# Optimization experiments

Measured on AMD Instinct MI355X. Metric: run time of the kernel, lower is better.

Reference implementation:

```python
import jax, jax.numpy as jnp
import numpy as np

D_HEAD = 64
NEG_INF = jnp.float32(-jnp.inf)


def setup_inputs() -> dict:
    key = jax.random.key(0)
    ks = jax.random.split(key, 6)
    B, S, D, N, H = 8, 1024, 768, 12, 64
    init = 0.02
    return {
        "normalized_resid_pre": jax.random.normal(ks[0], (B, S, D), jnp.float32),
        "W_Q": jax.random.normal(ks[1], (N, D, H), jnp.float32) * init,
        "W_K": jax.random.normal(ks[2], (N, D, H), jnp.float32) * init,
        "W_V": jax.random.normal(ks[3], (N, D, H), jnp.float32) * init,
        "W_O": jax.random.normal(ks[4], (N, H, D), jnp.float32) * init,
        "b_Q": jnp.zeros((N, H), jnp.float32),
        "b_K": jnp.zeros((N, H), jnp.float32),
        "b_V": jnp.zeros((N, H), jnp.float32),
        "b_O": jnp.zeros((D,), jnp.float32),
    }


def _causal_mask(attn_scores):
    # Faithful to the source: keep entries where triu(scores, 1) != scores
    # (i.e. lower triangle incl. diagonal), set the rest to -inf.
    return jnp.where(jnp.triu(attn_scores, k=1) != attn_scores, attn_scores, NEG_INF)


def reference(normalized_resid_pre, W_Q, W_K, W_V, W_O, b_Q, b_K, b_V, b_O):
    x = normalized_resid_pre  # [b, p, d]
    keys = jnp.einsum('bpd,ndh->bpnh', x, W_K) + b_K
    queries = jnp.einsum('bpd,ndh->bpnh', x, W_Q) + b_Q
    attn_scores = jnp.einsum('bknh,bqnh->bnqk', keys, queries)  # [b, n, s_q, s_k]
    attn_probs = jax.nn.softmax(_causal_mask(attn_scores / np.sqrt(D_HEAD)), axis=-1)
    values = jnp.einsum('bpd,ndh->bpnh', x, W_V) + b_V
    z = jnp.einsum('bknh,bnqk->bqnh', values, attn_probs)
    attn_out = jnp.einsum('bpnh,nhe->bpe', z, W_O) + b_O
    return attn_out
```

## Files before the change

kernel.cpp:

```cpp
#include <hip/hip_runtime.h>
#include <stdint.h>

typedef __attribute__((ext_vector_type(4))) float f32x4;
typedef __attribute__((ext_vector_type(8))) __bf16 bf16v8;
typedef __attribute__((ext_vector_type(8))) unsigned short u16x8;
typedef __attribute__((ext_vector_type(4))) unsigned short u16x4;
typedef unsigned short u16;

#define AS1 __attribute__((address_space(1)))
#define AS3 __attribute__((address_space(3)))

__device__ __forceinline__ u16 f2b(float f) {
  union { __bf16 h; u16 u; } c; c.h = (__bf16)f; return c.u;
}

__device__ __forceinline__ f32x4 mfma16(bf16v8 a, bf16v8 b, f32x4 c) {
  return __builtin_amdgcn_mfma_f32_16x16x32_bf16(a, b, c, 0, 0, 0);
}

__device__ __forceinline__ void gl_lds16(const void* g, void* l) {
  __builtin_amdgcn_global_load_lds((AS1 void*)g, (AS3 void*)l, 16, 0, 0);
}

__global__ __launch_bounds__(256) void pack_x_kernel(
    const float* __restrict__ x, u16* __restrict__ xb, int n8) {
  int i = blockIdx.x * 256 + threadIdx.x;
  if (i >= n8) return;
  const f32x4* p = (const f32x4*)(x + (size_t)i * 8);
  f32x4 a = p[0], b = p[1];
  u16x8 o;
  o[0] = f2b(a[0]); o[1] = f2b(a[1]); o[2] = f2b(a[2]); o[3] = f2b(a[3]);
  o[4] = f2b(b[0]); o[5] = f2b(b[1]); o[6] = f2b(b[2]); o[7] = f2b(b[3]);
  *(u16x8*)(xb + (size_t)i * 8) = o;
}

__global__ __launch_bounds__(256) void pack_w_kernel(
    const float* __restrict__ in, u16* __restrict__ out,
    int in_ns, int in_rs, int out_ns, int out_rs, float scale) {
  __shared__ float t[64][65];
  const int n = blockIdx.z;
  const int a0 = blockIdx.x * 64, b0 = blockIdx.y * 64;
  const int c = threadIdx.x & 63, w = threadIdx.x >> 6;
  const float* ip = in + (size_t)n * in_ns;
#pragma unroll
  for (int i = 0; i < 16; ++i) {
    int r = i * 4 + w;
    t[r][c] = ip[(size_t)(a0 + r) * in_rs + (b0 + c)];
  }
  __syncthreads();
  u16* op = out + (size_t)n * out_ns;
#pragma unroll
  for (int i = 0; i < 16; ++i) {
    int r = i * 4 + w;
    op[(size_t)(b0 + r) * out_rs + (a0 + c)] = f2b(t[c][r] * scale);
  }
}

__global__ __launch_bounds__(256) void pack_bias_kernel(
    const float* __restrict__ bq, const float* __restrict__ bk,
    float* __restrict__ o, float sq) {
  int i = blockIdx.x * 256 + threadIdx.x;
  if (i < 768) o[i] = bq[i] * sq;
  else if (i < 1536) o[i] = bk[i - 768];
}

template <int OUTF32, int BIASROW>
__global__ __launch_bounds__(256, 2) void gemm_bt(
    const u16* __restrict__ A, const u16* __restrict__ Bt,
    void* __restrict__ Cv, const float* __restrict__ bias, float scale, int N) {
  constexpr int K = 768;
  __shared__ u16 lA[2][128 * 32];
  __shared__ u16 lB[2][128 * 32];

  const int tid = threadIdx.x;
  const int lane = tid & 63, wid = tid >> 6;
  const int wr = wid >> 1, wc = wid & 1;
  const int g = lane >> 4, l16 = lane & 15;
  const int m0 = blockIdx.x * 128, n0 = blockIdx.y * 128;

  const int srow = tid >> 2;
  const int scol = (tid & 3) * 16;

  f32x4 acc[4][4];
#pragma unroll
  for (int i = 0; i < 4; ++i)
#pragma unroll
    for (int j = 0; j < 4; ++j) acc[i][j] = (f32x4)0.f;

  const char* Ab = (const char*)(A + (size_t)m0 * K);
  const char* Bb = (const char*)(Bt + (size_t)n0 * K);
  char* lAb = (char*)&lA[0][0];
  char* lBb = (char*)&lB[0][0];

#define STAGE(buf, kt)                                                          \
  do {                                                                          \
    int kb = (kt) * 64;                                                         \
    gl_lds16(Ab + (size_t)srow * 1536 + kb + scol,                              \
             lAb + (buf) * 8192 + wid * 1024);                                  \
    gl_lds16(Bb + (size_t)srow * 1536 + kb + scol,                              \
             lBb + (buf) * 8192 + wid * 1024);                                  \
    gl_lds16(Ab + (size_t)(64 + srow) * 1536 + kb + scol,                       \
             lAb + (buf) * 8192 + 4096 + wid * 1024);                           \
    gl_lds16(Bb + (size_t)(64 + srow) * 1536 + kb + scol,                       \
             lBb + (buf) * 8192 + 4096 + wid * 1024);                           \
  } while (0)

  STAGE(0, 0);
  __syncthreads();

  for (int kt = 0; kt < 24; ++kt) {
    const int cur = kt & 1;
    if (kt + 1 < 24) STAGE(cur ^ 1, kt + 1);
    bf16v8 af[4], bfv[4];
#pragma unroll
    for (int i = 0; i < 4; ++i) {
      af[i]  = *(const bf16v8*)&lA[cur][(wr * 64 + i * 16 + l16) * 32 + g * 8];
      bfv[i] = *(const bf16v8*)&lB[cur][(wc * 64 + i * 16 + l16) * 32 + g * 8];
    }
#pragma unroll
    for (int i = 0; i < 4; ++i)
#pragma unroll
      for (int j = 0; j < 4; ++j)
        acc[i][j] = mfma16(af[i], bfv[j], acc[i][j]);
    __syncthreads();
  }
#undef STAGE

  const int row0 = m0 + wr * 64, col0 = n0 + wc * 64;
#pragma unroll
  for (int j = 0; j < 4; ++j) {
    const int col = col0 + j * 16 + l16;
    const float bcol = BIASROW ? 0.f : bias[col];
#pragma unroll
    for (int i = 0; i < 4; ++i) {
#pragma unroll
      for (int r = 0; r < 4; ++r) {
        const int row = row0 + i * 16 + g * 4 + r;
        const float bv = BIASROW ? bias[row] : bcol;
        const float v = (acc[i][j][r] + bv) * scale;
        if (OUTF32) ((float*)Cv)[(size_t)row * N + col] = v;
        else        ((u16*)Cv)[(size_t)row * N + col] = f2b(v);
      }
    }
  }
}

__global__ __launch_bounds__(256, 3) void flash6_kernel(
    const u16* __restrict__ QK, const u16* __restrict__ Vt,
    u16* __restrict__ Z) {
  __shared__ u16 lK[2][64 * 64];
  __shared__ u16 lV[2][64 * 64];
  __shared__ u16 lP[64 * 72];

  const int tid = threadIdx.x;
  const int lane = tid & 63, wid = tid >> 6;
  const int g = lane >> 4, l16 = lane & 15;

  const int id = blockIdx.x;
  const int xs = id & 7;
  const int rest = id >> 3;
  const int p = rest & 7;
  const int j = rest >> 3;
  const int head = xs + 8 * j;
  const int b = head / 12, n = head % 12;

  const int nchA = 16 - p;
  const int total = 17;

  const u16* Qh = QK + (size_t)b * 1024 * 1536 + n * 64;
  const u16* Kh = Qh + 768;
  const u16* Vh = Vt + (size_t)n * 64 * 8192 + b * 1024;
  u16* Zh = Z + (size_t)b * 1024 * 768 + n * 64;
  u16* myP = &lP[(wid * 16) * 72];

  const int srow8 = lane >> 3;
  const int sslot = lane & 7;
  const int scol = ((sslot ^ srow8) << 4);

#define FSTAGE(buf, c)                                                        \
  do {                                                                        \
    const int kv0_ = (c) << 6;                                                \
    const char* kb_ = (const char*)Kh + (size_t)(kv0_ + (wid << 4)) * 3072;   \
    const char* vb_ = (const char*)Vh + (size_t)(wid << 4) * 16384 +          \
                      (size_t)kv0_ * 2;                                       \
    gl_lds16(kb_ + (size_t)srow8 * 3072 + scol,                               \
             (char*)&lK[buf][0] + (wid << 11));                               \
    gl_lds16(kb_ + (size_t)(8 + srow8) * 3072 + scol,                         \
             (char*)&lK[buf][0] + (wid << 11) + 1024);                        \
    gl_lds16(vb_ + (size_t)srow8 * 16384 + scol,                              \
             (char*)&lV[buf][0] + (wid << 11));                               \
    gl_lds16(vb_ + (size_t)(8 + srow8) * 16384 + scol,                        \
             (char*)&lV[buf][0] + (wid << 11) + 1024);                        \
  } while (0)

#define SWZ(row, slot) (((row) << 6) + ((((slot) ^ ((row) & 7))) << 3))

  const int qwA = (15 - p) * 64 + wid * 16;
  const int qwB = p * 64 + wid * 16;
  bf16v8 qfA[2], qfB[2];
#pragma unroll
  for (int kk = 0; kk < 2; ++kk) {
    qfA[kk] = *(const bf16v8*)(Qh + (size_t)(qwA + l16) * 1536 + kk * 32 + g * 8);
    qfB[kk] = *(const bf16v8*)(Qh + (size_t)(qwB + l16) * 1536 + kk * 32 + g * 8);
  }

  f32x4 po[4];
#pragma unroll
  for (int ht = 0; ht < 4; ++ht) po[ht] = (f32x4)0.f;
  float m = -3e38f, l = 0.f;

  FSTAGE(0, 0);
  __syncthreads();

  for (int s = 0; s < total; ++s) {
    const int cur = s & 1;
    const bool phB = s >= nchA;
    const int c = phB ? s - nchA : s;
    const int kv0 = c << 6;
    const int qw = phB ? qwB : qwA;

    if (s + 1 < total) {
      const int s1 = s + 1;
      const int c1 = (s1 >= nchA) ? s1 - nchA : s1;
      FSTAGE(cur ^ 1, c1);
    }

    const bf16v8 q0 = phB ? qfB[0] : qfA[0];
    const bf16v8 q1 = phB ? qfB[1] : qfA[1];

    bf16v8 kf[4][2];
#pragma unroll
    for (int kvt = 0; kvt < 4; ++kvt)
#pragma unroll
      for (int kk = 0; kk < 2; ++kk)
        kf[kvt][kk] =
            *(const bf16v8*)&lK[cur][SWZ(kvt * 16 + l16, kk * 4 + g)];
    f32x4 s_[4];
#pragma unroll
    for (int kvt = 0; kvt < 4; ++kvt) {
      f32x4 a = (f32x4)0.f;
      a = mfma16(kf[kvt][0], q0, a);
      a = mfma16(kf[kvt][1], q1, a);
      s_[kvt] = a;
    }
    bf16v8 vf[4][2];
#pragma unroll
    for (int ht = 0; ht < 4; ++ht)
#pragma unroll
      for (int kk = 0; kk < 2; ++kk)
        vf[ht][kk] =
            *(const bf16v8*)&lV[cur][SWZ(ht * 16 + l16, kk * 4 + g)];

    if (kv0 + 63 > qw) {
      const int qq = qw + l16;
#pragma unroll
      for (int kvt = 0; kvt < 4; ++kvt) {
        const int kv = kv0 + kvt * 16 + g * 4;
#pragma unroll
        for (int r = 0; r < 4; ++r)
          if (kv + r > qq) s_[kvt][r] = -3e38f;
      }
    }
    {
      float cm = s_[0][0];
#pragma unroll
      for (int kvt = 0; kvt < 4; ++kvt)
#pragma unroll
        for (int r = 0; r < 4; ++r) cm = fmaxf(cm, s_[kvt][r]);
      cm = fmaxf(cm, __shfl_xor(cm, 16));
      cm = fmaxf(cm, __shfl_xor(cm, 32));
      const float mn = fmaxf(m, cm);
      const float scl = exp2f(m - mn);
      m = mn;
      float rs = 0.f;
#pragma unroll
      for (int kvt = 0; kvt < 4; ++kvt) {
        u16x4 pw;
#pragma unroll
        for (int r = 0; r < 4; ++r) {
          const float pv = exp2f(s_[kvt][r] - mn);
          rs += pv;
          pw[r] = f2b(pv);
        }
        *(u16x4*)&myP[l16 * 72 + kvt * 16 + g * 4] = pw;
      }
      rs += __shfl_xor(rs, 16);
      rs += __shfl_xor(rs, 32);
      l = l * scl + rs;
#pragma unroll
      for (int r = 0; r < 4; ++r) {
        const float sr = __shfl(scl, g * 4 + r);
#pragma unroll
        for (int ht = 0; ht < 4; ++ht) po[ht][r] *= sr;
      }
    }
    bf16v8 pa[2];
#pragma unroll
    for (int kk = 0; kk < 2; ++kk)
      pa[kk] = *(const bf16v8*)&myP[l16 * 72 + kk * 32 + g * 8];
#pragma unroll
    for (int ht = 0; ht < 4; ++ht) {
      po[ht] = mfma16(pa[0], vf[ht][0], po[ht]);
      po[ht] = mfma16(pa[1], vf[ht][1], po[ht]);
    }

    __syncthreads();

    if (s == nchA - 1 || s == total - 1) {
#pragma unroll
      for (int r = 0; r < 4; ++r) {
        const float lr = __shfl(l, g * 4 + r);
        const float inv = 1.f / lr;
        const int qq = qw + g * 4 + r;
#pragma unroll
        for (int ht = 0; ht < 4; ++ht)
          Zh[(size_t)qq * 768 + ht * 16 + l16] = f2b(po[ht][r] * inv);
      }
      m = -3e38f;
      l = 0.f;
#pragma unroll
      for (int ht = 0; ht < 4; ++ht) po[ht] = (f32x4)0.f;
    }
  }
#undef FSTAGE
#undef SWZ
}

extern "C" void kernel_launch(void* const* d_in, const int* in_sizes, int n_in,
                              void* d_out, int out_size, void* d_ws,
                              size_t ws_size, hipStream_t stream) {
  const float* x  = (const float*)d_in[0];
  const float* wq = (const float*)d_in[1];
  const float* wk = (const float*)d_in[2];
  const float* wv = (const float*)d_in[3];
  const float* wo = (const float*)d_in[4];
  const float* bq = (const float*)d_in[5];
  const float* bk = (const float*)d_in[6];
  const float* bv = (const float*)d_in[7];
  const float* bo = (const float*)d_in[8];
  float* out = (float*)d_out;

  const float sq = 0.18033688011112042f;

  char* ws = (char*)d_ws;
  u16* Xb   = (u16*)ws; ws += 12582912;
  u16* BtQK = (u16*)ws; ws += 2359296;
  u16* WvT  = (u16*)ws; ws += 1179648;
  u16* WoT  = (u16*)ws; ws += 1179648;
  float* bc = (float*)ws; ws += 6144;
  u16* QKb  = (u16*)ws; ws += 25165824;
  u16* Vtb  = (u16*)ws; ws += 12582912;
  u16* Zb   = (u16*)ws; ws += 12582912;

  pack_x_kernel<<<3072, 256, 0, stream>>>(x, Xb, 786432);
  pack_w_kernel<<<dim3(12, 1, 12), 256, 0, stream>>>(wq, BtQK, 49152, 64,
                                                     49152, 768, sq);
  pack_w_kernel<<<dim3(12, 1, 12), 256, 0, stream>>>(wk, BtQK + 589824, 49152,
                                                     64, 49152, 768, 1.0f);
  pack_w_kernel<<<dim3(12, 1, 12), 256, 0, stream>>>(wv, WvT, 49152, 64,
                                                     49152, 768, 1.0f);
  pack_w_kernel<<<dim3(1, 12, 12), 256, 0, stream>>>(wo, WoT, 49152, 768,
                                                     64, 768, 1.0f);
  pack_bias_kernel<<<6, 256, 0, stream>>>(bq, bk, bc, sq);

  gemm_bt<0, 0><<<dim3(64, 12), 256, 0, stream>>>(Xb, BtQK, QKb, bc, 1.0f,
                                                  1536);
  gemm_bt<0, 1><<<dim3(6, 64), 256, 0, stream>>>(WvT, Xb, Vtb, bv, 1.0f, 8192);

  flash6_kernel<<<dim3(768), 256, 0, stream>>>(QKb, Vtb, Zb);

  gemm_bt<1, 0><<<dim3(64, 6), 256, 0, stream>>>(Zb, WoT, out, bo, 1.0f, 768);
}
```

Before: 131.4 us.

## Merge pack kernels, add narrow-tile GEMM variant, and defer softmax rescaling

Folds the bias packing into the x-pack kernel and merges the four weight-transpose launches into one, cutting six small launches down to two. Adds a TN=64 tile option to the GEMM so the V and output projections run with more blocks (384→768) and a higher occupancy hint. In the flash kernel, rescaling of the running max and accumulator is skipped whenever the new block max exceeds the old one by at most 8 (log2 units), which avoids shuffles and multiplies at the risk of larger intermediate values in bf16 P.

```diff
diff --git a/kernel.cpp b/kernel.cpp
--- a/kernel.cpp
+++ b/kernel.cpp
@@ -23,25 +23,44 @@
 }
 
 __global__ __launch_bounds__(256) void pack_x_kernel(
-    const float* __restrict__ x, u16* __restrict__ xb, int n8) {
+    const float* __restrict__ x, u16* __restrict__ xb, int n8,
+    const float* __restrict__ bq, const float* __restrict__ bk,
+    float* __restrict__ bc, float sq) {
   int i = blockIdx.x * 256 + threadIdx.x;
-  if (i >= n8) return;
-  const f32x4* p = (const f32x4*)(x + (size_t)i * 8);
-  f32x4 a = p[0], b = p[1];
-  u16x8 o;
-  o[0] = f2b(a[0]); o[1] = f2b(a[1]); o[2] = f2b(a[2]); o[3] = f2b(a[3]);
-  o[4] = f2b(b[0]); o[5] = f2b(b[1]); o[6] = f2b(b[2]); o[7] = f2b(b[3]);
-  *(u16x8*)(xb + (size_t)i * 8) = o;
-}
-
-__global__ __launch_bounds__(256) void pack_w_kernel(
-    const float* __restrict__ in, u16* __restrict__ out,
-    int in_ns, int in_rs, int out_ns, int out_rs, float scale) {
+  if (i < n8) {
+    const f32x4* p = (const f32x4*)(x + (size_t)i * 8);
+    f32x4 a = p[0], b = p[1];
+    u16x8 o;
+    o[0] = f2b(a[0]); o[1] = f2b(a[1]); o[2] = f2b(a[2]); o[3] = f2b(a[3]);
+    o[4] = f2b(b[0]); o[5] = f2b(b[1]); o[6] = f2b(b[2]); o[7] = f2b(b[3]);
+    *(u16x8*)(xb + (size_t)i * 8) = o;
+  } else {
+    int j = i - n8;
+    if (j < 768) bc[j] = bq[j] * sq;
+    else if (j < 1536) bc[j] = bk[j - 768];
+  }
+}
+
+__global__ __launch_bounds__(256) void pack_w_all(
+    const float* __restrict__ wq, const float* __restrict__ wk,
+    const float* __restrict__ wv, const float* __restrict__ wo,
+    u16* __restrict__ btqk, u16* __restrict__ wvt, u16* __restrict__ wot,
+    float sq) {
   __shared__ float t[64][65];
-  const int n = blockIdx.z;
-  const int a0 = blockIdx.x * 64, b0 = blockIdx.y * 64;
+  const int z = blockIdx.z;
+  const int which = z / 12, n = z % 12;
   const int c = threadIdx.x & 63, w = threadIdx.x >> 6;
-  const float* ip = in + (size_t)n * in_ns;
+
+  const float* in; u16* out; int in_rs, out_ns; float scale;
+  int a0, b0;
+  if (which == 0) { in = wq; out = btqk;          in_rs = 64;  out_ns = 49152; scale = sq;  }
+  else if (which == 1) { in = wk; out = btqk + 589824; in_rs = 64; out_ns = 49152; scale = 1.f; }
+  else if (which == 2) { in = wv; out = wvt;      in_rs = 64;  out_ns = 49152; scale = 1.f; }
+  else { in = wo; out = wot;                      in_rs = 768; out_ns = 64;    scale = 1.f; }
+  if (which < 3) { a0 = blockIdx.x * 64; b0 = 0; }
+  else           { a0 = 0; b0 = blockIdx.x * 64; }
+
+  const float* ip = in + (size_t)n * 49152;
 #pragma unroll
   for (int i = 0; i < 16; ++i) {
     int r = i * 4 + w;
@@ -52,38 +71,33 @@
 #pragma unroll
   for (int i = 0; i < 16; ++i) {
     int r = i * 4 + w;
-    op[(size_t)(b0 + r) * out_rs + (a0 + c)] = f2b(t[c][r] * scale);
-  }
-}
-
-__global__ __launch_bounds__(256) void pack_bias_kernel(
-    const float* __restrict__ bq, const float* __restrict__ bk,
-    float* __restrict__ o, float sq) {
-  int i = blockIdx.x * 256 + threadIdx.x;
-  if (i < 768) o[i] = bq[i] * sq;
-  else if (i < 1536) o[i] = bk[i - 768];
-}
-
-template <int OUTF32, int BIASROW>
-__global__ __launch_bounds__(256, 2) void gemm_bt(
+    op[(size_t)(b0 + r) * 768 + (a0 + c)] = f2b(t[c][r] * scale);
+  }
+}
+
+template <int OUTF32, int BIASROW, int TN>
+__global__ __launch_bounds__(256, 3) void gemm_bt(
     const u16* __restrict__ A, const u16* __restrict__ Bt,
     void* __restrict__ Cv, const float* __restrict__ bias, float scale, int N) {
   constexpr int K = 768;
+  constexpr int MI = (TN == 128) ? 4 : 2;
   __shared__ u16 lA[2][128 * 32];
-  __shared__ u16 lB[2][128 * 32];
+  __shared__ u16 lB[2][TN * 32];
+  constexpr int BBUF = TN * 64;
 
   const int tid = threadIdx.x;
   const int lane = tid & 63, wid = tid >> 6;
-  const int wr = wid >> 1, wc = wid & 1;
   const int g = lane >> 4, l16 = lane & 15;
-  const int m0 = blockIdx.x * 128, n0 = blockIdx.y * 128;
+  const int rowb = (TN == 128) ? (wid >> 1) * 64 : wid * 32;
+  const int colb = (TN == 128) ? (wid & 1) * 64 : 0;
+  const int m0 = blockIdx.x * 128, n0 = blockIdx.y * TN;
 
   const int srow = tid >> 2;
   const int scol = (tid & 3) * 16;
 
-  f32x4 acc[4][4];
-#pragma unroll
-  for (int i = 0; i < 4; ++i)
+  f32x4 acc[MI][4];
+#pragma unroll
+  for (int i = 0; i < MI; ++i)
 #pragma unroll
     for (int j = 0; j < 4; ++j) acc[i][j] = (f32x4)0.f;
 
@@ -97,12 +111,17 @@
     int kb = (kt) * 64;                                                         \
     gl_lds16(Ab + (size_t)srow * 1536 + kb + scol,                              \
              lAb + (buf) * 8192 + wid * 1024);                                  \
-    gl_lds16(Bb + (size_t)srow * 1536 + kb + scol,                              \
-             lBb + (buf) * 8192 + wid * 1024);                                  \
     gl_lds16(Ab + (size_t)(64 + srow) * 1536 + kb + scol,                       \
              lAb + (buf) * 8192 + 4096 + wid * 1024);                           \
-    gl_lds16(Bb + (size_t)(64 + srow) * 1536 + kb + scol,                       \
-             lBb + (buf) * 8192 + 4096 + wid * 1024);                           \
+    if (TN == 128) {                                                            \
+      gl_lds16(Bb + (size_t)srow * 1536 + kb + scol,                            \
+               lBb + (buf) * BBUF + wid * 1024);                                \
+      gl_lds16(Bb + (size_t)(64 + srow) * 1536 + kb + scol,                     \
+               lBb + (buf) * BBUF + 4096 + wid * 1024);                         \
+    } else if (srow < 64) {                                                     \
+      gl_lds16(Bb + (size_t)srow * 1536 + kb + scol,                            \
+               lBb + (buf) * BBUF + wid * 1024);                                \
+    }                                                                           \
   } while (0)
 
   STAGE(0, 0);
@@ -111,14 +130,15 @@
   for (int kt = 0; kt < 24; ++kt) {
     const int cur = kt & 1;
     if (kt + 1 < 24) STAGE(cur ^ 1, kt + 1);
-    bf16v8 af[4], bfv[4];
-#pragma unroll
-    for (int i = 0; i < 4; ++i) {
-      af[i]  = *(const bf16v8*)&lA[cur][(wr * 64 + i * 16 + l16) * 32 + g * 8];
-      bfv[i] = *(const bf16v8*)&lB[cur][(wc * 64 + i * 16 + l16) * 32 + g * 8];
-    }
-#pragma unroll
-    for (int i = 0; i < 4; ++i)
+    bf16v8 af[MI], bfv[4];
+#pragma unroll
+    for (int i = 0; i < MI; ++i)
+      af[i] = *(const bf16v8*)&lA[cur][(rowb + i * 16 + l16) * 32 + g * 8];
+#pragma unroll
+    for (int j = 0; j < 4; ++j)
+      bfv[j] = *(const bf16v8*)&lB[cur][(colb + j * 16 + l16) * 32 + g * 8];
+#pragma unroll
+    for (int i = 0; i < MI; ++i)
 #pragma unroll
       for (int j = 0; j < 4; ++j)
         acc[i][j] = mfma16(af[i], bfv[j], acc[i][j]);
@@ -126,13 +146,13 @@
   }
 #undef STAGE
 
-  const int row0 = m0 + wr * 64, col0 = n0 + wc * 64;
+  const int row0 = m0 + rowb, col0 = n0 + colb;
 #pragma unroll
   for (int j = 0; j < 4; ++j) {
     const int col = col0 + j * 16 + l16;
     const float bcol = BIASROW ? 0.f : bias[col];
 #pragma unroll
-    for (int i = 0; i < 4; ++i) {
+    for (int i = 0; i < MI; ++i) {
 #pragma unroll
       for (int r = 0; r < 4; ++r) {
         const int row = row0 + i * 16 + g * 4 + r;
@@ -269,16 +289,26 @@
         for (int r = 0; r < 4; ++r) cm = fmaxf(cm, s_[kvt][r]);
       cm = fmaxf(cm, __shfl_xor(cm, 16));
       cm = fmaxf(cm, __shfl_xor(cm, 32));
-      const float mn = fmaxf(m, cm);
-      const float scl = exp2f(m - mn);
-      m = mn;
+      const bool defer = __all(cm - m <= 8.0f);
+      float scl = 1.0f;
+      if (!defer) {
+        const float mn = fmaxf(m, cm);
+        scl = exp2f(m - mn);
+        m = mn;
+#pragma unroll
+        for (int r = 0; r < 4; ++r) {
+          const float sr = __shfl(scl, g * 4 + r);
+#pragma unroll
+          for (int ht = 0; ht < 4; ++ht) po[ht][r] *= sr;
+        }
+      }
       float rs = 0.f;
 #pragma unroll
       for (int kvt = 0; kvt < 4; ++kvt) {
         u16x4 pw;
 #pragma unroll
         for (int r = 0; r < 4; ++r) {
-          const float pv = exp2f(s_[kvt][r] - mn);
+          const float pv = exp2f(s_[kvt][r] - m);
           rs += pv;
           pw[r] = f2b(pv);
         }
@@ -287,12 +317,6 @@
       rs += __shfl_xor(rs, 16);
       rs += __shfl_xor(rs, 32);
       l = l * scl + rs;
-#pragma unroll
-      for (int r = 0; r < 4; ++r) {
-        const float sr = __shfl(scl, g * 4 + r);
-#pragma unroll
-        for (int ht = 0; ht < 4; ++ht) po[ht][r] *= sr;
-      }
     }
     bf16v8 pa[2];
 #pragma unroll
@@ -352,22 +376,17 @@
   u16* Vtb  = (u16*)ws; ws += 12582912;
   u16* Zb   = (u16*)ws; ws += 12582912;
 
-  pack_x_kernel<<<3072, 256, 0, stream>>>(x, Xb, 786432);
-  pack_w_kernel<<<dim3(12, 1, 12), 256, 0, stream>>>(wq, BtQK, 49152, 64,
-                                                     49152, 768, sq);
-  pack_w_kernel<<<dim3(12, 1, 12), 256, 0, stream>>>(wk, BtQK + 589824, 49152,
-                                                     64, 49152, 768, 1.0f);
-  pack_w_kernel<<<dim3(12, 1, 12), 256, 0, stream>>>(wv, WvT, 49152, 64,
-                                                     49152, 768, 1.0f);
-  pack_w_kernel<<<dim3(1, 12, 12), 256, 0, stream>>>(wo, WoT, 49152, 768,
-                                                     64, 768, 1.0f);
-  pack_bias_kernel<<<6, 256, 0, stream>>>(bq, bk, bc, sq);
-
-  gemm_bt<0, 0><<<dim3(64, 12), 256, 0, stream>>>(Xb, BtQK, QKb, bc, 1.0f,
-                                                  1536);
-  gemm_bt<0, 1><<<dim3(6, 64), 256, 0, stream>>>(WvT, Xb, Vtb, bv, 1.0f, 8192);
+  pack_x_kernel<<<3078, 256, 0, stream>>>(x, Xb, 786432, bq, bk, bc, sq);
+  pack_w_all<<<dim3(12, 1, 48), 256, 0, stream>>>(wq, wk, wv, wo, BtQK, WvT,
+                                                  WoT, sq);
+
+  gemm_bt<0, 0, 128><<<dim3(64, 12), 256, 0, stream>>>(Xb, BtQK, QKb, bc,
+                                                       1.0f, 1536);
+  gemm_bt<0, 1, 64><<<dim3(6, 128), 256, 0, stream>>>(WvT, Xb, Vtb, bv, 1.0f,
+                                                      8192);
 
   flash6_kernel<<<dim3(768), 256, 0, stream>>>(QKb, Vtb, Zb);
 
-  gemm_bt<1, 0><<<dim3(64, 6), 256, 0, stream>>>(Zb, WoT, out, bo, 1.0f, 768);
-}
+  gemm_bt<1, 0, 64><<<dim3(64, 12), 256, 0, stream>>>(Zb, WoT, out, bo, 1.0f,
+                                                      768);
+}
```

Result: faster. 119.7 us (-9.0%).
